# Kernel tuning notes

Hardware: AMD Instinct MI355X
Metric: run time of the kernel (lower is better)

Reference implementation:

```python
import jax, jax.numpy as jnp
import numpy as np

N, M, D = 1024, 1024, 256

def setup_inputs() -> dict:
    key = jax.random.key(0)
    ks = jax.random.split(key, 10)
    s = 1.0 / np.sqrt(D)
    return {
        "f_r": jax.random.normal(ks[0], (N, D), jnp.float32),
        "f_r_prime": jax.random.normal(ks[1], (M, D), jnp.float32),
        "W_w": jax.random.uniform(ks[2], (D, D), jnp.float32, -s, s),
        "W_b": jax.random.uniform(ks[3], (D,), jnp.float32, -s, s),
        "Wp_w": jax.random.uniform(ks[4], (D, D), jnp.float32, -s, s),
        "Wp_b": jax.random.uniform(ks[5], (D,), jnp.float32, -s, s),
        "w_w": jax.random.uniform(ks[6], (1, D), jnp.float32, -s, s),
        "w_b": jax.random.uniform(ks[7], (1,), jnp.float32, -s, s),
        "wp_w": jax.random.uniform(ks[8], (1, D), jnp.float32, -s, s),
        "wp_b": jax.random.uniform(ks[9], (1,), jnp.float32, -s, s),
    }

def reference(f_r, f_r_prime, W_w, W_b, Wp_w, Wp_b, w_w, w_b, wp_w, wp_b):
    q = f_r @ W_w.T + W_b            # [N, D]
    k = f_r_prime @ Wp_w.T + Wp_b    # [M, D]
    # additive (Bahdanau) scores: tanh over broadcast sum [N, M, D]
    h = jnp.tanh(q[:, None, :] + k[None, :, :])
    alpha = h @ w_w.T + w_b          # [N, M, 1]
    alpha = jax.nn.softmax(alpha, axis=1)
    # stage-1 pooling over M (weights on raw f_r_prime, as in source)
    context = jnp.sum(alpha * f_r_prime[None, :, :], axis=1)  # [N, D]
    # stage-2 attention pooling over N
    alpha_p = jax.nn.softmax(context @ wp_w.T + wp_b, axis=0)  # [N, 1]
    pool = jnp.sum(alpha_p * context, axis=0, keepdims=True)   # [1, D]
    return pool
```

## Files before the change

kernel.cpp:

```cpp
#include <hip/hip_runtime.h>

#define NN 1024
#define MM 1024
#define DD 256

typedef float floatx2 __attribute__((ext_vector_type(2)));

__device__ __forceinline__ float rcp_fast(float x) { return __builtin_amdgcn_rcpf(x); }

__global__ __launch_bounds__(256) void gemm_exp_kernel(
    const float* __restrict__ f_r,  const float* __restrict__ W_w,  const float* __restrict__ W_b,
    const float* __restrict__ f_rp, const float* __restrict__ Wp_w, const float* __restrict__ Wp_b,
    float* __restrict__ Eq, float* __restrict__ EkT, float* __restrict__ out0)
{
    __shared__ float As[32][36];
    __shared__ float Bs[32][68];
    __shared__ float T[64][36];

    const int b = blockIdx.x;
    const int t = threadIdx.x;
    if (b == 0) out0[t] = 0.f;

    const int mat  = b >> 7;
    const int tile = b & 127;
    const int rt = tile & 31, dt = tile >> 5;
    const float* __restrict__ A    = mat ? f_rp : f_r;
    const float* __restrict__ B    = mat ? Wp_w : W_w;
    const float* __restrict__ bias = mat ? Wp_b : W_b;

    const int tx = t & 15, ty = t >> 4;
    const int r0 = rt * 32, d0 = dt * 64;
    const int ar = t >> 3, ak = (t & 7) * 4;
    const int br = t >> 2, bk = (t & 3) * 8;

    float acc[2][4];
    #pragma unroll
    for (int i = 0; i < 2; ++i)
        #pragma unroll
        for (int j = 0; j < 4; ++j) acc[i][j] = 0.f;

    for (int kk = 0; kk < DD; kk += 32) {
        float4 av  = *(const float4*)(A + (size_t)(r0 + ar) * DD + kk + ak);
        float4 bv0 = *(const float4*)(B + (size_t)(d0 + br) * DD + kk + bk);
        float4 bv1 = *(const float4*)(B + (size_t)(d0 + br) * DD + kk + bk + 4);
        __syncthreads();
        As[ak + 0][ar] = av.x; As[ak + 1][ar] = av.y; As[ak + 2][ar] = av.z; As[ak + 3][ar] = av.w;
        Bs[bk + 0][br] = bv0.x; Bs[bk + 1][br] = bv0.y; Bs[bk + 2][br] = bv0.z; Bs[bk + 3][br] = bv0.w;
        Bs[bk + 4][br] = bv1.x; Bs[bk + 5][br] = bv1.y; Bs[bk + 6][br] = bv1.z; Bs[bk + 7][br] = bv1.w;
        __syncthreads();
        #pragma unroll
        for (int k = 0; k < 32; ++k) {
            float2 a2 = *(const float2*)&As[k][ty * 2];
            float4 b4 = *(const float4*)&Bs[k][tx * 4];
            float aa[2] = {a2.x, a2.y};
            float bb[4] = {b4.x, b4.y, b4.z, b4.w};
            #pragma unroll
            for (int i = 0; i < 2; ++i)
                #pragma unroll
                for (int j = 0; j < 4; ++j)
                    acc[i][j] = fmaf(aa[i], bb[j], acc[i][j]);
        }
    }

    float bj[4];
    #pragma unroll
    for (int j = 0; j < 4; ++j) bj[j] = bias[d0 + tx * 4 + j];

    float e[2][4];
    #pragma unroll
    for (int i = 0; i < 2; ++i)
        #pragma unroll
        for (int j = 0; j < 4; ++j) {
            float v = acc[i][j] + bj[j];
            v = fminf(fmaxf(v, -5.f), 5.f);
            e[i][j] = __expf(2.f * v);
        }

    if (mat == 0) {
        #pragma unroll
        for (int i = 0; i < 2; ++i)
            *(float4*)&Eq[(size_t)(r0 + ty * 2 + i) * DD + d0 + tx * 4] =
                make_float4(e[i][0], e[i][1], e[i][2], e[i][3]);
    } else {
        __syncthreads();
        #pragma unroll
        for (int i = 0; i < 2; ++i)
            #pragma unroll
            for (int j = 0; j < 4; ++j) T[tx * 4 + j][ty * 2 + i] = e[i][j];
        __syncthreads();
        const int dl = t >> 3, rl = (t & 7) * 4;
        #pragma unroll
        for (int h = 0; h < 2; ++h) {
            int dloc = dl + 32 * h;
            float4 tv = *(const float4*)&T[dloc][rl];
            *(float4*)&EkT[(size_t)(d0 + dloc) * MM + r0 + rl] = tv;
        }
    }
}

__global__ __launch_bounds__(1024, 4) void fused_attn_kernel(
    const float* __restrict__ Eq, const float* __restrict__ EkT,
    const float* __restrict__ w_w, const float* __restrict__ frp,
    const float* __restrict__ wp_w,
    float* __restrict__ ctx, float* __restrict__ score)
{
    __shared__ float accbuf[4][16][256];
    __shared__ float alsm[4][MM];
    __shared__ float4 ctxred[16][4][64];
    __shared__ float redmx[4][4];
    __shared__ float redsm[4][4];
    __shared__ float redsc[16];

    const int t  = threadIdx.x;
    const int tg = t >> 8;
    const int tm = t & 255;
    const int n0 = blockIdx.x * 4;

    const int dh = __builtin_amdgcn_readfirstlane(tg * 64);
    const float* __restrict__ eqb = Eq + (size_t)n0 * DD + dh;
    const float* __restrict__ wwb = w_w + dh;

    const floatx2 one2 = {1.f, 1.f};
    floatx2 accl[4] = {{0.f,0.f},{0.f,0.f},{0.f,0.f},{0.f,0.f}};
    floatx2 acch[4] = {{0.f,0.f},{0.f,0.f},{0.f,0.f},{0.f,0.f}};

    const float* ekb = EkT + (size_t)dh * MM + 4 * tm;
    float4 c0 = *(const float4*)(ekb + 0 * MM);
    float4 c1 = *(const float4*)(ekb + 1 * MM);
    float4 c2 = *(const float4*)(ekb + 2 * MM);
    float4 c3 = *(const float4*)(ekb + 3 * MM);

    for (int gi = 0; gi < 16; ++gi) {
        float4 p0 = c0, p1 = c1, p2 = c2, p3 = c3;
        if (gi < 15) {
            const float* nb = ekb + (size_t)(gi * 4 + 4) * MM;
            p0 = *(const float4*)(nb + 0 * MM);
            p1 = *(const float4*)(nb + 1 * MM);
            p2 = *(const float4*)(nb + 2 * MM);
            p3 = *(const float4*)(nb + 3 * MM);
        }
        const int db = gi * 4;
        float4 w4 = *(const float4*)(wwb + db);
        floatx2 kv[4][2] = {{{c0.x, c0.y}, {c0.z, c0.w}},
                            {{c1.x, c1.y}, {c1.z, c1.w}},
                            {{c2.x, c2.y}, {c2.z, c2.w}},
                            {{c3.x, c3.y}, {c3.z, c3.w}}};
        #pragma unroll
        for (int n = 0; n < 4; ++n) {
            float4 q4 = *(const float4*)(eqb + n * DD + db);
            #pragma unroll
            for (int h = 0; h < 2; ++h) {
                floatx2 x0 = q4.x * kv[0][h] + one2;
                floatx2 x1 = q4.y * kv[1][h] + one2;
                floatx2 x2 = q4.z * kv[2][h] + one2;
                floatx2 x3 = q4.w * kv[3][h] + one2;
                floatx2 p01 = x0 * x1;
                floatx2 p23 = x2 * x3;
                floatx2 n01 = w4.x * x1 + w4.y * x0;
                floatx2 n23 = w4.z * x3 + w4.w * x2;
                floatx2 nc  = n01 * p23 + n23 * p01;
                floatx2 pt  = p01 * p23;
                floatx2 r;  r.x = rcp_fast(pt.x);  r.y = rcp_fast(pt.y);
                if (h == 0) accl[n] += nc * r; else acch[n] += nc * r;
            }
        }
        c0 = p0; c1 = p1; c2 = p2; c3 = p3;
    }

    float acc[4][4];
    #pragma unroll
    for (int n = 0; n < 4; ++n) {
        acc[n][0] = -2.f * accl[n].x; acc[n][1] = -2.f * accl[n].y;
        acc[n][2] = -2.f * acch[n].x; acc[n][3] = -2.f * acch[n].y;
    }

    #pragma unroll
    for (int n = 0; n < 4; ++n)
        #pragma unroll
        for (int j = 0; j < 4; ++j) accbuf[tg][n * 4 + j][tm] = acc[n][j];
    __syncthreads();

    const int g = tg;
    const int w4id = (t >> 6) & 3;
    const int lane = t & 63;
    float aj[4];
    #pragma unroll
    for (int j = 0; j < 4; ++j)
        aj[j] = accbuf[0][g * 4 + j][tm] + accbuf[1][g * 4 + j][tm]
              + accbuf[2][g * 4 + j][tm] + accbuf[3][g * 4 + j][tm];

    float mx = fmaxf(fmaxf(aj[0], aj[1]), fmaxf(aj[2], aj[3]));
    #pragma unroll
    for (int off = 32; off > 0; off >>= 1) mx = fmaxf(mx, __shfl_xor(mx, off));
    if (lane == 0) redmx[g][w4id] = mx;
    __syncthreads();
    const float MX = fmaxf(fmaxf(redmx[g][0], redmx[g][1]), fmaxf(redmx[g][2], redmx[g][3]));

    float e[4], sm = 0.f;
    #pragma unroll
    for (int j = 0; j < 4; ++j) { e[j] = __expf(aj[j] - MX); sm += e[j]; }
    #pragma unroll
    for (int off = 32; off > 0; off >>= 1) sm += __shfl_xor(sm, off);
    if (lane == 0) redsm[g][w4id] = sm;
    __syncthreads();
    const float S = redsm[g][0] + redsm[g][1] + redsm[g][2] + redsm[g][3];
    const float inv = rcp_fast(S);
    *(float4*)&alsm[g][4 * tm] = make_float4(e[0] * inv, e[1] * inv, e[2] * inv, e[3] * inv);
    __syncthreads();

    const int cc = t & 63;
    const int rr = t >> 6;
    const int m0 = rr * 64;
    floatx2 axl[4] = {{0.f,0.f},{0.f,0.f},{0.f,0.f},{0.f,0.f}};
    floatx2 axh[4] = {{0.f,0.f},{0.f,0.f},{0.f,0.f},{0.f,0.f}};
    const float* fb = frp + (size_t)m0 * DD + 4 * cc;
    for (int m4 = 0; m4 < 16; ++m4) {
        float alv[4][4];
        #pragma unroll
        for (int n = 0; n < 4; ++n) {
            float4 a4 = *(const float4*)&alsm[n][m0 + m4 * 4];
            alv[n][0] = a4.x; alv[n][1] = a4.y; alv[n][2] = a4.z; alv[n][3] = a4.w;
        }
        #pragma unroll
        for (int mm = 0; mm < 4; ++mm) {
            float4 f = *(const float4*)(fb + (size_t)(m4 * 4 + mm) * DD);
            floatx2 fl = {f.x, f.y}, fh = {f.z, f.w};
            #pragma unroll
            for (int n = 0; n < 4; ++n) {
                axl[n] += alv[n][mm] * fl;
                axh[n] += alv[n][mm] * fh;
            }
        }
    }
    #pragma unroll
    for (int n = 0; n < 4; ++n)
        ctxred[rr][n][cc] = make_float4(axl[n].x, axl[n].y, axh[n].x, axh[n].y);
    __syncthreads();

    const int nn = t >> 8, d = t & 255;
    float s = 0.f;
    #pragma unroll
    for (int r = 0; r < 16; ++r)
        s += ((const float*)&ctxred[r][nn][d >> 2])[d & 3];
    ctx[(size_t)(n0 + nn) * DD + d] = s;

    float p = s * wp_w[d];
    #pragma unroll
    for (int off = 32; off > 0; off >>= 1) p += __shfl_xor(p, off);
    if (lane == 0) redsc[t >> 6] = p;
    __syncthreads();
    if (t < 4) score[n0 + t] = redsc[4 * t] + redsc[4 * t + 1] + redsc[4 * t + 2] + redsc[4 * t + 3];
}

__global__ __launch_bounds__(256) void pool_kernel(
    const float* __restrict__ ctx, const float* __restrict__ score,
    float* __restrict__ out)
{
    __shared__ float red[8];
    const int t = threadIdx.x, lane = t & 63, wid = t >> 6;
    const int n0 = blockIdx.x * 4;

    float s0 = score[t], s1 = score[t + 256], s2 = score[t + 512], s3 = score[t + 768];
    float mx = fmaxf(fmaxf(s0, s1), fmaxf(s2, s3));
    #pragma unroll
    for (int off = 32; off > 0; off >>= 1) mx = fmaxf(mx, __shfl_xor(mx, off));
    if (lane == 0) red[wid] = mx;
    __syncthreads();
    mx = fmaxf(fmaxf(red[0], red[1]), fmaxf(red[2], red[3]));

    float se = __expf(s0 - mx) + __expf(s1 - mx) + __expf(s2 - mx) + __expf(s3 - mx);
    #pragma unroll
    for (int off = 32; off > 0; off >>= 1) se += __shfl_xor(se, off);
    if (lane == 0) red[4 + wid] = se;
    __syncthreads();
    se = red[4] + red[5] + red[6] + red[7];
    float invS = rcp_fast(se);

    float r = 0.f;
    #pragma unroll
    for (int i = 0; i < 4; ++i) {
        float ap = __expf(score[n0 + i] - mx) * invS;
        r = fmaf(ap, ctx[(size_t)(n0 + i) * DD + t], r);
    }
    atomicAdd(out + t, r);
}

extern "C" void kernel_launch(void* const* d_in, const int* in_sizes, int n_in,
                              void* d_out, int out_size, void* d_ws, size_t ws_size,
                              hipStream_t stream) {
    const float* f_r  = (const float*)d_in[0];
    const float* f_rp = (const float*)d_in[1];
    const float* W_w  = (const float*)d_in[2];
    const float* W_b  = (const float*)d_in[3];
    const float* Wp_w = (const float*)d_in[4];
    const float* Wp_b = (const float*)d_in[5];
    const float* w_w  = (const float*)d_in[6];
    const float* wp_w = (const float*)d_in[8];
    float* out = (float*)d_out;

    float* ws    = (float*)d_ws;
    float* Eq    = ws;
    float* EkT   = ws + 262144;
    float* ctx   = ws + 524288;
    float* score = ws + 786432;

    gemm_exp_kernel<<<256, 256, 0, stream>>>(f_r, W_w, W_b, f_rp, Wp_w, Wp_b, Eq, EkT, out);
    fused_attn_kernel<<<256, 1024, 0, stream>>>(Eq, EkT, w_w, f_rp, wp_w, ctx, score);
    pool_kernel<<<256, 256, 0, stream>>>(ctx, score, out);
}
```

Before: 124.5 us.

## Split attention over M into two halves with max-free softmax and combine kernel

The fused attention kernel now splits each row group's M range into two halves, launching twice as many blocks with half the per-thread work and a smaller shared-memory footprint so more blocks can be resident. Softmax drops the max subtraction and relies on tanh-bounded scores, writing partial unnormalized contexts and exp sums that a new combine kernel adds, normalizes and scores. This trades one extra kernel launch and extra global traffic for more parallelism and occupancy.

Result: slower. 127.6 us (+2.5%).

```diff
diff --git a/kernel.cpp b/kernel.cpp
--- a/kernel.cpp
+++ b/kernel.cpp
@@ -98,132 +98,109 @@
     }
 }
 
-__global__ __launch_bounds__(1024, 4) void fused_attn_kernel(
+__global__ __launch_bounds__(1024, 8) void fused_attn_kernel(
     const float* __restrict__ Eq, const float* __restrict__ EkT,
     const float* __restrict__ w_w, const float* __restrict__ frp,
-    const float* __restrict__ wp_w,
-    float* __restrict__ ctx, float* __restrict__ score)
+    float* __restrict__ ctxA, float* __restrict__ ctxB,
+    float* __restrict__ SpA, float* __restrict__ SpB)
 {
-    __shared__ float accbuf[4][16][256];
-    __shared__ float alsm[4][MM];
-    __shared__ float4 ctxred[16][4][64];
-    __shared__ float redmx[4][4];
+    __shared__ __align__(16) char usm_raw[65536];
+    float2 (*accbuf)[4][256] = (float2 (*)[4][256])(void*)usm_raw;
+    float4 (*ctxred)[4][64]  = (float4 (*)[4][64])(void*)usm_raw;
+    __shared__ float alsm[4][512];
     __shared__ float redsm[4][4];
-    __shared__ float redsc[16];
 
     const int t  = threadIdx.x;
     const int tg = t >> 8;
     const int tm = t & 255;
-    const int n0 = blockIdx.x * 4;
+    const int bm = blockIdx.x & 1;
+    const int n0 = (blockIdx.x >> 1) * 4;
+    const int m0 = bm * 512;
 
     const int dh = __builtin_amdgcn_readfirstlane(tg * 64);
     const float* __restrict__ eqb = Eq + (size_t)n0 * DD + dh;
     const float* __restrict__ wwb = w_w + dh;
 
     const floatx2 one2 = {1.f, 1.f};
-    floatx2 accl[4] = {{0.f,0.f},{0.f,0.f},{0.f,0.f},{0.f,0.f}};
-    floatx2 acch[4] = {{0.f,0.f},{0.f,0.f},{0.f,0.f},{0.f,0.f}};
-
-    const float* ekb = EkT + (size_t)dh * MM + 4 * tm;
-    float4 c0 = *(const float4*)(ekb + 0 * MM);
-    float4 c1 = *(const float4*)(ekb + 1 * MM);
-    float4 c2 = *(const float4*)(ekb + 2 * MM);
-    float4 c3 = *(const float4*)(ekb + 3 * MM);
+    floatx2 acc2[4] = {{0.f,0.f},{0.f,0.f},{0.f,0.f},{0.f,0.f}};
+
+    const float* ekb = EkT + (size_t)dh * MM + m0 + 2 * tm;
+    float2 c0 = *(const float2*)(ekb + 0 * MM);
+    float2 c1 = *(const float2*)(ekb + 1 * MM);
+    float2 c2 = *(const float2*)(ekb + 2 * MM);
+    float2 c3 = *(const float2*)(ekb + 3 * MM);
 
     for (int gi = 0; gi < 16; ++gi) {
-        float4 p0 = c0, p1 = c1, p2 = c2, p3 = c3;
+        float2 p0 = c0, p1 = c1, p2 = c2, p3 = c3;
         if (gi < 15) {
             const float* nb = ekb + (size_t)(gi * 4 + 4) * MM;
-            p0 = *(const float4*)(nb + 0 * MM);
-            p1 = *(const float4*)(nb + 1 * MM);
-            p2 = *(const float4*)(nb + 2 * MM);
-            p3 = *(const float4*)(nb + 3 * MM);
+            p0 = *(const float2*)(nb + 0 * MM);
+            p1 = *(const float2*)(nb + 1 * MM);
+            p2 = *(const float2*)(nb + 2 * MM);
+            p3 = *(const float2*)(nb + 3 * MM);
         }
         const int db = gi * 4;
         float4 w4 = *(const float4*)(wwb + db);
-        floatx2 kv[4][2] = {{{c0.x, c0.y}, {c0.z, c0.w}},
-                            {{c1.x, c1.y}, {c1.z, c1.w}},
-                            {{c2.x, c2.y}, {c2.z, c2.w}},
-                            {{c3.x, c3.y}, {c3.z, c3.w}}};
+        floatx2 kv0 = {c0.x, c0.y}, kv1 = {c1.x, c1.y};
+        floatx2 kv2 = {c2.x, c2.y}, kv3 = {c3.x, c3.y};
         #pragma unroll
         for (int n = 0; n < 4; ++n) {
             float4 q4 = *(const float4*)(eqb + n * DD + db);
-            #pragma unroll
-            for (int h = 0; h < 2; ++h) {
-                floatx2 x0 = q4.x * kv[0][h] + one2;
-                floatx2 x1 = q4.y * kv[1][h] + one2;
-                floatx2 x2 = q4.z * kv[2][h] + one2;
-                floatx2 x3 = q4.w * kv[3][h] + one2;
-                floatx2 p01 = x0 * x1;
-                floatx2 p23 = x2 * x3;
-                floatx2 n01 = w4.x * x1 + w4.y * x0;
-                floatx2 n23 = w4.z * x3 + w4.w * x2;
-                floatx2 nc  = n01 * p23 + n23 * p01;
-                floatx2 pt  = p01 * p23;
-                floatx2 r;  r.x = rcp_fast(pt.x);  r.y = rcp_fast(pt.y);
-                if (h == 0) accl[n] += nc * r; else acch[n] += nc * r;
-            }
+            floatx2 x0 = q4.x * kv0 + one2;
+            floatx2 x1 = q4.y * kv1 + one2;
+            floatx2 x2 = q4.z * kv2 + one2;
+            floatx2 x3 = q4.w * kv3 + one2;
+            floatx2 p01 = x0 * x1;
+            floatx2 p23 = x2 * x3;
+            floatx2 n01 = w4.x * x1 + w4.y * x0;
+            floatx2 n23 = w4.z * x3 + w4.w * x2;
+            floatx2 nc  = n01 * p23 + n23 * p01;
+            floatx2 pt  = p01 * p23;
+            floatx2 r;  r.x = rcp_fast(pt.x);  r.y = rcp_fast(pt.y);
+            acc2[n] += nc * r;
         }
         c0 = p0; c1 = p1; c2 = p2; c3 = p3;
     }
 
-    float acc[4][4];
-    #pragma unroll
-    for (int n = 0; n < 4; ++n) {
-        acc[n][0] = -2.f * accl[n].x; acc[n][1] = -2.f * accl[n].y;
-        acc[n][2] = -2.f * acch[n].x; acc[n][3] = -2.f * acch[n].y;
-    }
-
     #pragma unroll
     for (int n = 0; n < 4; ++n)
-        #pragma unroll
-        for (int j = 0; j < 4; ++j) accbuf[tg][n * 4 + j][tm] = acc[n][j];
+        accbuf[tg][n][tm] = make_float2(-2.f * acc2[n].x, -2.f * acc2[n].y);
     __syncthreads();
 
     const int g = tg;
     const int w4id = (t >> 6) & 3;
     const int lane = t & 63;
-    float aj[4];
-    #pragma unroll
-    for (int j = 0; j < 4; ++j)
-        aj[j] = accbuf[0][g * 4 + j][tm] + accbuf[1][g * 4 + j][tm]
-              + accbuf[2][g * 4 + j][tm] + accbuf[3][g * 4 + j][tm];
-
-    float mx = fmaxf(fmaxf(aj[0], aj[1]), fmaxf(aj[2], aj[3]));
-    #pragma unroll
-    for (int off = 32; off > 0; off >>= 1) mx = fmaxf(mx, __shfl_xor(mx, off));
-    if (lane == 0) redmx[g][w4id] = mx;
-    __syncthreads();
-    const float MX = fmaxf(fmaxf(redmx[g][0], redmx[g][1]), fmaxf(redmx[g][2], redmx[g][3]));
-
-    float e[4], sm = 0.f;
-    #pragma unroll
-    for (int j = 0; j < 4; ++j) { e[j] = __expf(aj[j] - MX); sm += e[j]; }
+    float2 a0 = accbuf[0][g][tm], a1 = accbuf[1][g][tm];
+    float2 a2 = accbuf[2][g][tm], a3 = accbuf[3][g][tm];
+    float sx = a0.x + a1.x + a2.x + a3.x;
+    float sy = a0.y + a1.y + a2.y + a3.y;
+    float ex = __expf(sx), ey = __expf(sy);
+    *(float2*)&alsm[g][2 * tm] = make_float2(ex, ey);
+    float sm = ex + ey;
     #pragma unroll
     for (int off = 32; off > 0; off >>= 1) sm += __shfl_xor(sm, off);
     if (lane == 0) redsm[g][w4id] = sm;
     __syncthreads();
-    const float S = redsm[g][0] + redsm[g][1] + redsm[g][2] + redsm[g][3];
-    const float inv = rcp_fast(S);
-    *(float4*)&alsm[g][4 * tm] = make_float4(e[0] * inv, e[1] * inv, e[2] * inv, e[3] * inv);
-    __syncthreads();
+    if (tm == 0) {
+        float* Sp = bm ? SpB : SpA;
+        Sp[n0 + g] = redsm[g][0] + redsm[g][1] + redsm[g][2] + redsm[g][3];
+    }
 
     const int cc = t & 63;
     const int rr = t >> 6;
-    const int m0 = rr * 64;
     floatx2 axl[4] = {{0.f,0.f},{0.f,0.f},{0.f,0.f},{0.f,0.f}};
     floatx2 axh[4] = {{0.f,0.f},{0.f,0.f},{0.f,0.f},{0.f,0.f}};
-    const float* fb = frp + (size_t)m0 * DD + 4 * cc;
-    for (int m4 = 0; m4 < 16; ++m4) {
+    const float* fb = frp + (size_t)(m0 + rr * 32) * DD + 4 * cc;
+    for (int m8 = 0; m8 < 8; ++m8) {
         float alv[4][4];
         #pragma unroll
         for (int n = 0; n < 4; ++n) {
-            float4 a4 = *(const float4*)&alsm[n][m0 + m4 * 4];
+            float4 a4 = *(const float4*)&alsm[n][rr * 32 + m8 * 4];
             alv[n][0] = a4.x; alv[n][1] = a4.y; alv[n][2] = a4.z; alv[n][3] = a4.w;
         }
         #pragma unroll
         for (int mm = 0; mm < 4; ++mm) {
-            float4 f = *(const float4*)(fb + (size_t)(m4 * 4 + mm) * DD);
+            float4 f = *(const float4*)(fb + (size_t)(m8 * 4 + mm) * DD);
             floatx2 fl = {f.x, f.y}, fh = {f.z, f.w};
             #pragma unroll
             for (int n = 0; n < 4; ++n) {
@@ -242,14 +219,30 @@
     #pragma unroll
     for (int r = 0; r < 16; ++r)
         s += ((const float*)&ctxred[r][nn][d >> 2])[d & 3];
-    ctx[(size_t)(n0 + nn) * DD + d] = s;
-
-    float p = s * wp_w[d];
-    #pragma unroll
-    for (int off = 32; off > 0; off >>= 1) p += __shfl_xor(p, off);
-    if (lane == 0) redsc[t >> 6] = p;
-    __syncthreads();
-    if (t < 4) score[n0 + t] = redsc[4 * t] + redsc[4 * t + 1] + redsc[4 * t + 2] + redsc[4 * t + 3];
+    float* ctxP = bm ? ctxB : ctxA;
+    ctxP[(size_t)(n0 + nn) * DD + d] = s;
+}
+
+__global__ __launch_bounds__(256) void combine_kernel(
+    const float* __restrict__ ctxA, const float* __restrict__ ctxB,
+    const float* __restrict__ SpA, const float* __restrict__ SpB,
+    const float* __restrict__ wp_w,
+    float* __restrict__ ctx, float* __restrict__ score)
+{
+    const int t = threadIdx.x, lane = t & 63;
+    const int row = blockIdx.x * 4 + (t >> 6);
+    const float inv = rcp_fast(SpA[row] + SpB[row]);
+    const size_t off = (size_t)row * DD + 4 * lane;
+    float4 a = *(const float4*)(ctxA + off);
+    float4 b = *(const float4*)(ctxB + off);
+    float4 c = make_float4((a.x + b.x) * inv, (a.y + b.y) * inv,
+                           (a.z + b.z) * inv, (a.w + b.w) * inv);
+    *(float4*)(ctx + off) = c;
+    float4 w = *(const float4*)(wp_w + 4 * lane);
+    float p = c.x * w.x + c.y * w.y + c.z * w.z + c.w * w.w;
+    #pragma unroll
+    for (int o = 32; o > 0; o >>= 1) p += __shfl_xor(p, o);
+    if (lane == 0) score[row] = p;
 }
 
 __global__ __launch_bounds__(256) void pool_kernel(
@@ -301,10 +294,15 @@
     float* ws    = (float*)d_ws;
     float* Eq    = ws;
     float* EkT   = ws + 262144;
-    float* ctx   = ws + 524288;
-    float* score = ws + 786432;
+    float* ctxA  = ws + 524288;
+    float* ctxB  = ws + 786432;
+    float* ctxn  = ws + 1048576;
+    float* SpA   = ws + 1310720;
+    float* SpB   = ws + 1311744;
+    float* score = ws + 1312768;
 
     gemm_exp_kernel<<<256, 256, 0, stream>>>(f_r, W_w, W_b, f_rp, Wp_w, Wp_b, Eq, EkT, out);
-    fused_attn_kernel<<<256, 1024, 0, stream>>>(Eq, EkT, w_w, f_rp, wp_w, ctx, score);
-    pool_kernel<<<256, 256, 0, stream>>>(ctx, score, out);
-}
+    fused_attn_kernel<<<512, 1024, 0, stream>>>(Eq, EkT, w_w, f_rp, ctxA, ctxB, SpA, SpB);
+    combine_kernel<<<256, 256, 0, stream>>>(ctxA, ctxB, SpA, SpB, wp_w, ctxn, score);
+    pool_kernel<<<256, 256, 0, stream>>>(ctxn, score, out);
+}
```

## Split attention over M into two halves and merge partial softmax in pool kernel

Applied to the files above, without the earlier changes.

The fused attention kernel now launches twice as many blocks, with each block handling half of the M dimension. Instead of normalizing locally, each block writes unnormalized partial context, partial exp-sum and partial score, and the pool kernel combines the halves and divides by the summed denominator. The max subtraction is dropped because the tanh-bounded scores keep exp in range, and shared memory is aliased between the accumulator and reduction buffers to allow higher occupancy. The aim is to fill more compute units and cut per-block serial work, at the cost of extra workspace traffic and a heavier merge step.

New measurement: 122.7 us. Within noise of the previous version (-1.5%).

```diff
diff --git a/kernel.cpp b/kernel.cpp
--- a/kernel.cpp
+++ b/kernel.cpp
@@ -98,25 +98,29 @@
     }
 }
 
-__global__ __launch_bounds__(1024, 4) void fused_attn_kernel(
+__global__ __launch_bounds__(1024, 8) void fused_attn_kernel(
     const float* __restrict__ Eq, const float* __restrict__ EkT,
     const float* __restrict__ w_w, const float* __restrict__ frp,
     const float* __restrict__ wp_w,
-    float* __restrict__ ctx, float* __restrict__ score)
+    float* __restrict__ ctxA, float* __restrict__ ctxB,
+    float* __restrict__ SpA, float* __restrict__ SpB,
+    float* __restrict__ sA,  float* __restrict__ sB)
 {
-    __shared__ float accbuf[4][16][256];
-    __shared__ float alsm[4][MM];
-    __shared__ float4 ctxred[16][4][64];
-    __shared__ float redmx[4][4];
+    __shared__ __align__(16) char usm_raw[65536];
+    float2 (*accbuf2)[4][256] = (float2 (*)[4][256])(void*)usm_raw;
+    float4 (*ctxred)[4][64]   = (float4 (*)[4][64])(void*)usm_raw;
+    __shared__ float alsm[4][512];
     __shared__ float redsm[4][4];
     __shared__ float redsc[16];
 
     const int t  = threadIdx.x;
-    const int tg = t >> 8;
-    const int tm = t & 255;
-    const int n0 = blockIdx.x * 4;
-
-    const int dh = __builtin_amdgcn_readfirstlane(tg * 64);
+    const int tg = t >> 7;
+    const int tm = t & 127;
+    const int bm = blockIdx.x & 1;
+    const int n0 = (blockIdx.x >> 1) * 4;
+    const int m0 = bm * 512;
+
+    const int dh = __builtin_amdgcn_readfirstlane(tg * 32);
     const float* __restrict__ eqb = Eq + (size_t)n0 * DD + dh;
     const float* __restrict__ wwb = w_w + dh;
 
@@ -124,21 +128,14 @@
     floatx2 accl[4] = {{0.f,0.f},{0.f,0.f},{0.f,0.f},{0.f,0.f}};
     floatx2 acch[4] = {{0.f,0.f},{0.f,0.f},{0.f,0.f},{0.f,0.f}};
 
-    const float* ekb = EkT + (size_t)dh * MM + 4 * tm;
-    float4 c0 = *(const float4*)(ekb + 0 * MM);
-    float4 c1 = *(const float4*)(ekb + 1 * MM);
-    float4 c2 = *(const float4*)(ekb + 2 * MM);
-    float4 c3 = *(const float4*)(ekb + 3 * MM);
-
-    for (int gi = 0; gi < 16; ++gi) {
-        float4 p0 = c0, p1 = c1, p2 = c2, p3 = c3;
-        if (gi < 15) {
-            const float* nb = ekb + (size_t)(gi * 4 + 4) * MM;
-            p0 = *(const float4*)(nb + 0 * MM);
-            p1 = *(const float4*)(nb + 1 * MM);
-            p2 = *(const float4*)(nb + 2 * MM);
-            p3 = *(const float4*)(nb + 3 * MM);
-        }
+    const float* ekb = EkT + (size_t)dh * MM + m0 + 4 * tm;
+
+    for (int gi = 0; gi < 8; ++gi) {
+        const float* nb = ekb + (size_t)(gi * 4) * MM;
+        float4 c0 = *(const float4*)(nb + 0 * MM);
+        float4 c1 = *(const float4*)(nb + 1 * MM);
+        float4 c2 = *(const float4*)(nb + 2 * MM);
+        float4 c3 = *(const float4*)(nb + 3 * MM);
         const int db = gi * 4;
         float4 w4 = *(const float4*)(wwb + db);
         floatx2 kv[4][2] = {{{c0.x, c0.y}, {c0.z, c0.w}},
@@ -164,66 +161,50 @@
                 if (h == 0) accl[n] += nc * r; else acch[n] += nc * r;
             }
         }
-        c0 = p0; c1 = p1; c2 = p2; c3 = p3;
-    }
-
-    float acc[4][4];
-    #pragma unroll
-    for (int n = 0; n < 4; ++n) {
-        acc[n][0] = -2.f * accl[n].x; acc[n][1] = -2.f * accl[n].y;
-        acc[n][2] = -2.f * acch[n].x; acc[n][3] = -2.f * acch[n].y;
     }
 
     #pragma unroll
     for (int n = 0; n < 4; ++n)
-        #pragma unroll
-        for (int j = 0; j < 4; ++j) accbuf[tg][n * 4 + j][tm] = acc[n][j];
-    __syncthreads();
-
-    const int g = tg;
+        *(float4*)&accbuf2[tg][n][2 * tm] =
+            make_float4(accl[n].x, accl[n].y, acch[n].x, acch[n].y);
+    __syncthreads();
+
+    const int bn = t >> 8, j = t & 255;
     const int w4id = (t >> 6) & 3;
     const int lane = t & 63;
-    float aj[4];
-    #pragma unroll
-    for (int j = 0; j < 4; ++j)
-        aj[j] = accbuf[0][g * 4 + j][tm] + accbuf[1][g * 4 + j][tm]
-              + accbuf[2][g * 4 + j][tm] + accbuf[3][g * 4 + j][tm];
-
-    float mx = fmaxf(fmaxf(aj[0], aj[1]), fmaxf(aj[2], aj[3]));
-    #pragma unroll
-    for (int off = 32; off > 0; off >>= 1) mx = fmaxf(mx, __shfl_xor(mx, off));
-    if (lane == 0) redmx[g][w4id] = mx;
-    __syncthreads();
-    const float MX = fmaxf(fmaxf(redmx[g][0], redmx[g][1]), fmaxf(redmx[g][2], redmx[g][3]));
-
-    float e[4], sm = 0.f;
-    #pragma unroll
-    for (int j = 0; j < 4; ++j) { e[j] = __expf(aj[j] - MX); sm += e[j]; }
+    float2 aj = make_float2(0.f, 0.f);
+    #pragma unroll
+    for (int g8 = 0; g8 < 8; ++g8) {
+        float2 v = accbuf2[g8][bn][j];
+        aj.x += v.x; aj.y += v.y;
+    }
+    float ex = __expf(-2.f * aj.x), ey = __expf(-2.f * aj.y);
+    *(float2*)&alsm[bn][2 * j] = make_float2(ex, ey);
+    float sm = ex + ey;
     #pragma unroll
     for (int off = 32; off > 0; off >>= 1) sm += __shfl_xor(sm, off);
-    if (lane == 0) redsm[g][w4id] = sm;
-    __syncthreads();
-    const float S = redsm[g][0] + redsm[g][1] + redsm[g][2] + redsm[g][3];
-    const float inv = rcp_fast(S);
-    *(float4*)&alsm[g][4 * tm] = make_float4(e[0] * inv, e[1] * inv, e[2] * inv, e[3] * inv);
-    __syncthreads();
+    if (lane == 0) redsm[bn][w4id] = sm;
+    __syncthreads();
+    if (j == 0) {
+        float* Sp = bm ? SpB : SpA;
+        Sp[n0 + bn] = redsm[bn][0] + redsm[bn][1] + redsm[bn][2] + redsm[bn][3];
+    }
 
     const int cc = t & 63;
     const int rr = t >> 6;
-    const int m0 = rr * 64;
     floatx2 axl[4] = {{0.f,0.f},{0.f,0.f},{0.f,0.f},{0.f,0.f}};
     floatx2 axh[4] = {{0.f,0.f},{0.f,0.f},{0.f,0.f},{0.f,0.f}};
-    const float* fb = frp + (size_t)m0 * DD + 4 * cc;
-    for (int m4 = 0; m4 < 16; ++m4) {
+    const float* fb = frp + (size_t)(m0 + rr * 32) * DD + 4 * cc;
+    for (int m8 = 0; m8 < 8; ++m8) {
         float alv[4][4];
         #pragma unroll
         for (int n = 0; n < 4; ++n) {
-            float4 a4 = *(const float4*)&alsm[n][m0 + m4 * 4];
+            float4 a4 = *(const float4*)&alsm[n][rr * 32 + m8 * 4];
             alv[n][0] = a4.x; alv[n][1] = a4.y; alv[n][2] = a4.z; alv[n][3] = a4.w;
         }
         #pragma unroll
         for (int mm = 0; mm < 4; ++mm) {
-            float4 f = *(const float4*)(fb + (size_t)(m4 * 4 + mm) * DD);
+            float4 f = *(const float4*)(fb + (size_t)(m8 * 4 + mm) * DD);
             floatx2 fl = {f.x, f.y}, fh = {f.z, f.w};
             #pragma unroll
             for (int n = 0; n < 4; ++n) {
@@ -242,33 +223,44 @@
     #pragma unroll
     for (int r = 0; r < 16; ++r)
         s += ((const float*)&ctxred[r][nn][d >> 2])[d & 3];
-    ctx[(size_t)(n0 + nn) * DD + d] = s;
+    float* ctxP = bm ? ctxB : ctxA;
+    ctxP[(size_t)(n0 + nn) * DD + d] = s;
 
     float p = s * wp_w[d];
     #pragma unroll
     for (int off = 32; off > 0; off >>= 1) p += __shfl_xor(p, off);
     if (lane == 0) redsc[t >> 6] = p;
     __syncthreads();
-    if (t < 4) score[n0 + t] = redsc[4 * t] + redsc[4 * t + 1] + redsc[4 * t + 2] + redsc[4 * t + 3];
+    if (t < 4) {
+        float* sP = bm ? sB : sA;
+        sP[n0 + t] = redsc[4 * t] + redsc[4 * t + 1] + redsc[4 * t + 2] + redsc[4 * t + 3];
+    }
 }
 
 __global__ __launch_bounds__(256) void pool_kernel(
-    const float* __restrict__ ctx, const float* __restrict__ score,
+    const float* __restrict__ ctxA, const float* __restrict__ ctxB,
+    const float* __restrict__ SpA,  const float* __restrict__ SpB,
+    const float* __restrict__ sA,   const float* __restrict__ sB,
     float* __restrict__ out)
 {
     __shared__ float red[8];
     const int t = threadIdx.x, lane = t & 63, wid = t >> 6;
     const int n0 = blockIdx.x * 4;
 
-    float s0 = score[t], s1 = score[t + 256], s2 = score[t + 512], s3 = score[t + 768];
-    float mx = fmaxf(fmaxf(s0, s1), fmaxf(s2, s3));
+    float sc[4];
+    #pragma unroll
+    for (int i = 0; i < 4; ++i) {
+        int r = t + 256 * i;
+        sc[i] = (sA[r] + sB[r]) * rcp_fast(SpA[r] + SpB[r]);
+    }
+    float mx = fmaxf(fmaxf(sc[0], sc[1]), fmaxf(sc[2], sc[3]));
     #pragma unroll
     for (int off = 32; off > 0; off >>= 1) mx = fmaxf(mx, __shfl_xor(mx, off));
     if (lane == 0) red[wid] = mx;
     __syncthreads();
     mx = fmaxf(fmaxf(red[0], red[1]), fmaxf(red[2], red[3]));
 
-    float se = __expf(s0 - mx) + __expf(s1 - mx) + __expf(s2 - mx) + __expf(s3 - mx);
+    float se = __expf(sc[0] - mx) + __expf(sc[1] - mx) + __expf(sc[2] - mx) + __expf(sc[3] - mx);
     #pragma unroll
     for (int off = 32; off > 0; off >>= 1) se += __shfl_xor(se, off);
     if (lane == 0) red[4 + wid] = se;
@@ -276,13 +268,17 @@
     se = red[4] + red[5] + red[6] + red[7];
     float invS = rcp_fast(se);
 
-    float r = 0.f;
+    float racc = 0.f;
     #pragma unroll
     for (int i = 0; i < 4; ++i) {
-        float ap = __expf(score[n0 + i] - mx) * invS;
-        r = fmaf(ap, ctx[(size_t)(n0 + i) * DD + t], r);
-    }
-    atomicAdd(out + t, r);
+        int row = n0 + i;
+        float invRow = rcp_fast(SpA[row] + SpB[row]);
+        float scr = (sA[row] + sB[row]) * invRow;
+        float ap = __expf(scr - mx) * invS;
+        float cr = (ctxA[(size_t)row * DD + t] + ctxB[(size_t)row * DD + t]) * invRow;
+        racc = fmaf(ap, cr, racc);
+    }
+    atomicAdd(out + t, racc);
 }
 
 extern "C" void kernel_launch(void* const* d_in, const int* in_sizes, int n_in,
@@ -301,10 +297,15 @@
     float* ws    = (float*)d_ws;
     float* Eq    = ws;
     float* EkT   = ws + 262144;
-    float* ctx   = ws + 524288;
-    float* score = ws + 786432;
+    float* ctxA  = ws + 524288;
+    float* ctxB  = ws + 786432;
+    float* SpA   = ws + 1048576;
+    float* SpB   = ws + 1049600;
+    float* sA    = ws + 1050624;
+    float* sB    = ws + 1051648;
 
     gemm_exp_kernel<<<256, 256, 0, stream>>>(f_r, W_w, W_b, f_rp, Wp_w, Wp_b, Eq, EkT, out);
-    fused_attn_kernel<<<256, 1024, 0, stream>>>(Eq, EkT, w_w, f_rp, wp_w, ctx, score);
-    pool_kernel<<<256, 256, 0, stream>>>(ctx, score, out);
+    fused_attn_kernel<<<512, 1024, 0, stream>>>(Eq, EkT, w_w, f_rp, wp_w,
+                                                ctxA, ctxB, SpA, SpB, sA, sB);
+    pool_kernel<<<256, 256, 0, stream>>>(ctxA, ctxB, SpA, SpB, sA, sB, out);
 }
```
